# Performance work log

Hardware: AMD Instinct MI355X
Metric: run time of the kernel (lower is better)

Reference implementation:

```python
import jax, jax.numpy as jnp
import numpy as np

B, N, D, H = 1, 4096, 1024, 16
K = D // H
ROPE_BASE = 10000.0


def _rope_cos_sin(n, k, base, dtype):
    # GPT-NeoX style rotary embedding: inv_freq over even dims, emb = cat(freqs, freqs)
    inv_freq = 1.0 / (base ** (jnp.arange(0, k, 2, dtype=jnp.float32) / k))  # [K/2]
    pos = jnp.arange(n, dtype=jnp.float32)
    freqs = pos[:, None] * inv_freq[None, :]              # [N, K/2]
    emb = jnp.concatenate([freqs, freqs], axis=-1)        # [N, K]
    return jnp.cos(emb).astype(dtype), jnp.sin(emb).astype(dtype)


def _rotate_half(x):
    x1, x2 = jnp.split(x, 2, axis=-1)
    return jnp.concatenate([-x2, x1], axis=-1)


def setup_inputs() -> dict:
    key = jax.random.key(0)
    kx, kq, ko = jax.random.split(key, 3)
    x = jax.random.normal(kx, (B, N, D), dtype=jnp.float32)
    # torch Linear weights: [out_features, in_features], y = x @ W^T
    w_qkv = jax.random.normal(kq, (3 * H * K, D), dtype=jnp.float32) / np.sqrt(D)
    w_out = jax.random.normal(ko, (D, D), dtype=jnp.float32) / np.sqrt(D)
    return {"x": x, "w_qkv": w_qkv, "w_out": w_out}


def reference(x, w_qkv, w_out):
    b, n, d = x.shape
    qkv = jnp.einsum('bnd,ed->bne', x, w_qkv).reshape(b, n, 3, H, K)
    q, k, v = qkv[:, :, 0], qkv[:, :, 1], qkv[:, :, 2]   # [B, N, H, K]
    cos, sin = _rope_cos_sin(n, K, ROPE_BASE, x.dtype)    # [N, K]
    cos = cos[None, :, None, :]
    sin = sin[None, :, None, :]
    q = q * cos + _rotate_half(q) * sin
    k = k * cos + _rotate_half(k) * sin
    # explicit O(N^2) score matrix, as in the original module
    scores = jnp.einsum('bnhk,bmhk->bnhm', q, k) / np.sqrt(K).astype(x.dtype)
    causal_mask = jnp.tril(jnp.ones((n, n), dtype=bool))  # [N, M]
    scores = jnp.where(causal_mask[None, :, None, :], scores, jnp.finfo(x.dtype).min)
    probs = jax.nn.softmax(scores, axis=-1)
    attn = jnp.einsum('bnhm,bmhk->bnhk', probs, v).reshape(b, n, d)
    return jnp.einsum('bnd,ed->bne', attn, w_out)
```

## Files before the change

### kernel.cpp

```cpp
#include <hip/hip_runtime.h>
#include <hip/hip_bf16.h>
#include <math.h>

#define N_SEQ 4096
#define DIM   1024
#define NHEAD 16
#define HDIM  64
#define E3    3072

typedef short bf16x8 __attribute__((ext_vector_type(8)));
typedef float f32x4  __attribute__((ext_vector_type(4)));
typedef unsigned int u32;

#if __has_builtin(__builtin_amdgcn_exp2f)
#define EXP2(x) __builtin_amdgcn_exp2f(x)
#else
#define EXP2(x) exp2f(x)
#endif

__device__ __forceinline__ float bf2f(unsigned short u) {
    union { unsigned int i; float f; } x; x.i = ((unsigned int)u) << 16; return x.f;
}
__device__ __forceinline__ unsigned short f2bf(float f) {
    union { float f; unsigned int i; } x; x.f = f;
    unsigned int r = x.i + 0x7FFF + ((x.i >> 16) & 1);
    return (unsigned short)(r >> 16);
}
__device__ __forceinline__ unsigned short f2bf_fast(float f) {
    union { float f; unsigned int i; } x; x.f = f;
    return (unsigned short)((x.i + 0x8000u) >> 16);
}
__device__ __forceinline__ f32x4 mfma16(bf16x8 a, bf16x8 b, f32x4 c) {
    return __builtin_amdgcn_mfma_f32_16x16x32_bf16(a, b, c, 0, 0, 0);
}
__device__ __forceinline__ void gload_lds16(const unsigned short* g, unsigned short* l) {
    __builtin_amdgcn_global_load_lds(
        (const __attribute__((address_space(1))) u32*)g,
        (__attribute__((address_space(3))) u32*)l, 16, 0, 0);
}

__device__ __forceinline__ int probe_isf32(const unsigned short* __restrict__ X) {
    __shared__ int cnt;
    if (threadIdx.x == 0) cnt = 0;
    __syncthreads();
    int bad = 0;
    for (int i = threadIdx.x; i < 4096; i += 256) {
        float v = bf2f(X[i]);
        if (!(fabsf(v) < 1e10f)) bad = 1;
    }
    if (bad) atomicAdd(&cnt, 1);
    __syncthreads();
    return cnt > 0;
}

__global__ __launch_bounds__(256)
void prep_kernel(const void* __restrict__ X, const void* __restrict__ Wq,
                 const void* __restrict__ Wo,
                 unsigned short* __restrict__ Xb, unsigned short* __restrict__ Wqb,
                 unsigned short* __restrict__ Wob,
                 int* __restrict__ flag)
{
    const int isf32 = probe_isf32((const unsigned short*)X);
    if (blockIdx.x == 0 && threadIdx.x == 0) *flag = isf32;
    if (!isf32) return;

    const int nX4  = (N_SEQ * DIM) >> 2;
    const int nWq4 = (E3 * DIM) >> 2;
    const int nWo4 = (DIM * DIM) >> 2;
    const int total = nX4 + nWq4 + nWo4;
    const int stride = gridDim.x * blockDim.x;
    for (int i = blockIdx.x * blockDim.x + threadIdx.x; i < total; i += stride) {
        const float4* src; ushort4* dst; int j = i;
        if (j < nX4)                { src = (const float4*)X  + j;  dst = (ushort4*)Xb  + j; }
        else if ((j -= nX4) < nWq4) { src = (const float4*)Wq + j;  dst = (ushort4*)Wqb + j; }
        else { j -= nWq4;             src = (const float4*)Wo + j;  dst = (ushort4*)Wob + j; }
        float4 v = *src;
        ushort4 u;
        u.x = f2bf(v.x); u.y = f2bf(v.y); u.z = f2bf(v.z); u.w = f2bf(v.w);
        *dst = u;
    }
}

__global__ __launch_bounds__(256)
void qkv_mfma_kernel(const void* __restrict__ Xo, const unsigned short* __restrict__ Xc,
                     const void* __restrict__ Wo_, const unsigned short* __restrict__ Wc,
                     const int* __restrict__ flag,
                     unsigned short* __restrict__ Qf,
                     unsigned short* __restrict__ Kf,
                     unsigned short* __restrict__ Vf)
{
    __shared__ __align__(16) unsigned short SMEM[4][4096];

    const int isf32 = *flag;
    const unsigned short* Xb = isf32 ? Xc : (const unsigned short*)Xo;
    const unsigned short* Wb = isf32 ? Wc : (const unsigned short*)Wo_;

    const int tid  = threadIdx.x;
    const int lane = tid & 63;
    const int wave = tid >> 6;
    const int wr = wave >> 1, wc = wave & 1;
    const int lm = lane & 15, q4 = lane >> 4;
    const int rbase = blockIdx.y * 128;
    const int cbase = blockIdx.x * 128;

    const int srow = wave * 16 + (lane >> 2);
    const int scol = (lane & 3) * 8;

    const unsigned short* xsrc = Xb + (size_t)(rbase + srow) * DIM + scol;
    const unsigned short* wsrc = Wb + (size_t)(cbase + srow) * DIM + scol;
    const int la = (wr*64 + lm)*32 + q4*8;
    const int lb = (wc*64 + lm)*32 + q4*8;

    f32x4 acc[4][4];
    #pragma unroll
    for (int i = 0; i < 4; ++i)
        #pragma unroll
        for (int j = 0; j < 4; ++j) acc[i][j] = (f32x4){0.f, 0.f, 0.f, 0.f};

    #define QSTAGE(buf)                                                             \
        {                                                                           \
            _Pragma("unroll")                                                       \
            for (int j = 0; j < 2; ++j) {                                           \
                gload_lds16(xsrc + (size_t)j*64*DIM, &SMEM[buf][j*2048 + wave*512]);   \
                gload_lds16(wsrc + (size_t)j*64*DIM, &SMEM[2+buf][j*2048 + wave*512]); \
            }                                                                       \
            xsrc += 32; wsrc += 32;                                                 \
        }

    QSTAGE(0)
    for (int it = 0; it < DIM/32; ++it) {
        const int cur = it & 1;
        __syncthreads();
        if (it + 1 < DIM/32) QSTAGE(cur ^ 1)

        bf16x8 a[4], b[4];
        #pragma unroll
        for (int mi = 0; mi < 4; ++mi)
            a[mi] = *(const bf16x8*)&SMEM[cur][la + mi*512];
        #pragma unroll
        for (int ni = 0; ni < 4; ++ni)
            b[ni] = *(const bf16x8*)&SMEM[2+cur][lb + ni*512];
        #pragma unroll
        for (int mi = 0; mi < 4; ++mi)
            #pragma unroll
            for (int ni = 0; ni < 4; ++ni)
                acc[mi][ni] = mfma16(a[mi], b[ni], acc[mi][ni]);
    }
    #undef QSTAGE

    __syncthreads();

    const int ecol = cbase + wc * 64;
    const int part = ecol >> 10;
    const int h    = (ecol >> 6) & 15;
    unsigned short* ep = &SMEM[0][0] + wave*4096;

    if (part == 2) {
        #pragma unroll
        for (int mh = 0; mh < 2; ++mh) {
            #pragma unroll
            for (int mi2 = 0; mi2 < 2; ++mi2) {
                const int mi = mh*2 + mi2;
                #pragma unroll
                for (int r = 0; r < 4; ++r) {
                    const int n31 = mi2*16 + q4*4 + r;
                    #pragma unroll
                    for (int ni = 0; ni < 4; ++ni)
                        ep[(ni*16 + lm)*40 + n31] = f2bf(acc[mi][ni][r]);
                }
            }
            const int nb = rbase + wr*64 + mh*32;
            const size_t vb = (((size_t)h*128 + (nb >> 5)) << 11) + (size_t)lane*8;
            #pragma unroll
            for (int ni = 0; ni < 4; ++ni) {
                const bf16x8 fr = *(const bf16x8*)(ep + (ni*16 + lm)*40 + q4*8);
                *(bf16x8*)(Vf + vb + (size_t)ni*512) = fr;
            }
        }
    } else {
        unsigned short* dst = (part == 0) ? Qf : Kf;
        const float scl = (part == 0) ? 0.180336884f : 1.0f;
        const float inv0 = powf(10000.f, -((float)lm)        * (1.f/32.f));
        const float inv1 = powf(10000.f, -((float)(lm + 16)) * (1.f/32.f));
        #pragma unroll
        for (int mi = 0; mi < 4; ++mi) {
            const int tn = rbase + wr*64 + mi*16;
            #pragma unroll
            for (int r = 0; r < 4; ++r) {
                const int n = tn + q4*4 + r;
                float s0, c0, s1, c1;
                sincosf((float)n * inv0, &s0, &c0);
                sincosf((float)n * inv1, &s1, &c1);
                const int row = (q4*4 + r)*72;
                ep[row + lm]      = f2bf((acc[mi][0][r]*c0 - acc[mi][2][r]*s0) * scl);
                ep[row + lm + 16] = f2bf((acc[mi][1][r]*c1 - acc[mi][3][r]*s1) * scl);
                ep[row + lm + 32] = f2bf((acc[mi][2][r]*c0 + acc[mi][0][r]*s0) * scl);
                ep[row + lm + 48] = f2bf((acc[mi][3][r]*c1 + acc[mi][1][r]*s1) * scl);
            }
            const size_t tb = (((size_t)(h*256 + (tn >> 4))) << 10) + (size_t)lane*8;
            #pragma unroll
            for (int c = 0; c < 2; ++c) {
                const bf16x8 fr = *(const bf16x8*)(ep + lm*72 + c*32 + q4*8);
                *(bf16x8*)(dst + tb + (size_t)c*512) = fr;
            }
        }
    }
}

__global__ __launch_bounds__(256)
void attn_mfma_kernel(const unsigned short* __restrict__ Qf,
                      const unsigned short* __restrict__ Kf,
                      const unsigned short* __restrict__ Vf,
                      unsigned short* __restrict__ Attn)
{
    __shared__ __align__(16) unsigned short Ks[2][4096];
    __shared__ __align__(16) unsigned short Vs[2][4096];
    __shared__ __align__(16) unsigned short P16[4][16][72];

    const int tid  = threadIdx.x;
    const int lane = tid & 63;
    const int wave = tid >> 6;
    const int q4 = lane >> 4, lm = lane & 15;

    const int h  = blockIdx.x & 15;
    const int qb = blockIdx.x >> 4;
    const int q0 = (63 - qb) << 6;
    const int qw = q0 + (wave << 4);

    const size_t qbase = (((size_t)(h*256 + (qw >> 4))) << 10) + (size_t)lane * 8;
    const bf16x8 aq0 = *(const bf16x8*)(Qf + qbase);
    const bf16x8 aq1 = *(const bf16x8*)(Qf + qbase + 512);

    float l_part[4];
    f32x4 o[4];
    #pragma unroll
    for (int r = 0; r < 4; ++r) l_part[r] = 0.f;
    #pragma unroll
    for (int dc = 0; dc < 4; ++dc) o[dc] = (f32x4){0.f, 0.f, 0.f, 0.f};

    const unsigned short* sbase;
    unsigned short* db0;
    unsigned short* db1;
    {
        const int ch0 = (wave & 1) * 4;
        const size_t hb = ((size_t)h) << 18;
        sbase = ((wave < 2) ? Kf : Vf) + hb + ch0*512 + (size_t)lane*8;
        db0 = ((wave < 2) ? &Ks[0][0] : &Vs[0][0]) + ch0*512;
        db1 = ((wave < 2) ? &Ks[1][0] : &Vs[1][0]) + ch0*512;
    }
    unsigned short* pw  = &P16[wave][0][0];
    unsigned short* pwa = pw + (4*q4)*72 + lm;
    const unsigned short* par = pw + lm*72 + 8*q4;

    const int ntiles = (q0 >> 6) + 1;

    #define STAGE(dst)                                                         \
        {                                                                      \
            _Pragma("unroll")                                                  \
            for (int i = 0; i < 4; ++i)                                        \
                gload_lds16(sbase + i*512, (dst) + i*512);                     \
            sbase += 4096;                                                     \
        }

    STAGE(db0)

    for (int it = 0; it < ntiles; ++it) {
        const int kt = it << 6;
        const int cur = it & 1;

        __syncthreads();
        if (it + 1 < ntiles) STAGE(cur ? db0 : db1)

        const unsigned short* kc = &Ks[cur][lane*8];
        const unsigned short* vc = &Vs[cur][lane*8];

        f32x4 s[4];
        #pragma unroll
        for (int t = 0; t < 4; ++t) {
            const bf16x8 bk0 = *(const bf16x8*)(kc + t*1024);
            const bf16x8 bk1 = *(const bf16x8*)(kc + t*1024 + 512);
            f32x4 z = (f32x4){0.f, 0.f, 0.f, 0.f};
            z = mfma16(aq0, bk0, z);
            s[t] = mfma16(aq1, bk1, z);
        }

        if (kt + 63 > qw) {
            #pragma unroll
            for (int t = 0; t < 4; ++t) {
                const int key = kt + 16*t + lm;
                #pragma unroll
                for (int r = 0; r < 4; ++r)
                    if (key > qw + 4*q4 + r) s[t][r] = -INFINITY;
            }
        }

        #pragma unroll
        for (int t = 0; t < 4; ++t)
            #pragma unroll
            for (int r = 0; r < 4; ++r) {
                const float p = EXP2(s[t][r]);
                l_part[r] += p;
                pwa[r*72 + 16*t] = f2bf_fast(p);
            }

        const bf16x8 pa0 = *(const bf16x8*)(par);
        const bf16x8 pa1 = *(const bf16x8*)(par + 32);

        #pragma unroll
        for (int dc = 0; dc < 4; ++dc) {
            const bf16x8 bv0 = *(const bf16x8*)(vc + dc*512);
            const bf16x8 bv1 = *(const bf16x8*)(vc + 2048 + dc*512);
            o[dc] = mfma16(pa0, bv0, o[dc]);
            o[dc] = mfma16(pa1, bv1, o[dc]);
        }
    }
    #undef STAGE

    float inv[4];
    #pragma unroll
    for (int r = 0; r < 4; ++r) {
        float l = l_part[r];
        #pragma unroll
        for (int mk = 1; mk <= 8; mk <<= 1) l += __shfl_xor(l, mk);
        inv[r] = 1.f / l;
    }
    #pragma unroll
    for (int dc = 0; dc < 4; ++dc)
        #pragma unroll
        for (int r = 0; r < 4; ++r)
            Attn[(size_t)(qw + 4*q4 + r) * DIM + (h << 6) + 16*dc + lm] = f2bf(o[dc][r] * inv[r]);
}

__global__ __launch_bounds__(256)
void out_mfma_kernel(const unsigned short* __restrict__ Ab,
                     const void* __restrict__ Wo_, const unsigned short* __restrict__ Wc,
                     const int* __restrict__ flag,
                     void* __restrict__ Out)
{
    __shared__ unsigned short As[2][4096];
    __shared__ unsigned short Bs[2][2048];

    const int isf32 = *flag;
    const unsigned short* Wb = isf32 ? Wc : (const unsigned short*)Wo_;

    const int tid  = threadIdx.x;
    const int lane = tid & 63;
    const int wave = tid >> 6;
    const int lm = lane & 15, q4 = lane >> 4;
    const int rbase = blockIdx.y * 128;
    const int cbase = blockIdx.x * 64;

    const int srow16 = lane >> 2;
    const int scol = (lane & 3) * 8;

    const unsigned short* asrc = Ab + (size_t)(rbase + wave*32 + srow16) * DIM + scol;
    const unsigned short* bsrc = Wb + (size_t)(cbase + wave*16 + srow16) * DIM + scol;
    const int la = (wave*32 + lm)*32 + q4*8;
    const int lb = lm*32 + q4*8;

    f32x4 acc[2][4];
    #pragma unroll
    for (int i = 0; i < 2; ++i)
        #pragma unroll
        for (int j = 0; j < 4; ++j) acc[i][j] = (f32x4){0.f, 0.f, 0.f, 0.f};

    #define OSTAGE(buf)                                                          \
        {                                                                        \
            _Pragma("unroll")                                                    \
            for (int j = 0; j < 2; ++j)                                          \
                gload_lds16(asrc + (size_t)j*16*DIM, &As[buf][(wave*32 + j*16)*32]); \
            gload_lds16(bsrc, &Bs[buf][(wave*16)*32]);                           \
            asrc += 32; bsrc += 32;                                              \
        }

    OSTAGE(0)
    for (int it = 0; it < DIM/32; ++it) {
        const int cur = it & 1;
        __syncthreads();
        if (it + 1 < DIM/32) OSTAGE(cur ^ 1)

        bf16x8 a[2], b[4];
        #pragma unroll
        for (int mi = 0; mi < 2; ++mi)
            a[mi] = *(const bf16x8*)&As[cur][la + mi*512];
        #pragma unroll
        for (int ni = 0; ni < 4; ++ni)
            b[ni] = *(const bf16x8*)&Bs[cur][lb + ni*512];
        #pragma unroll
        for (int mi = 0; mi < 2; ++mi)
            #pragma unroll
            for (int ni = 0; ni < 4; ++ni)
                acc[mi][ni] = mfma16(a[mi], b[ni], acc[mi][ni]);
    }
    #undef OSTAGE

    #pragma unroll
    for (int mi = 0; mi < 2; ++mi)
        #pragma unroll
        for (int r = 0; r < 4; ++r) {
            const size_t n = rbase + wave*32 + mi*16 + q4*4 + r;
            #pragma unroll
            for (int ni = 0; ni < 4; ++ni) {
                const size_t e = cbase + ni*16 + lm;
                const float v = acc[mi][ni][r];
                if (isf32) ((float*)Out)[n * DIM + e] = v;
                else       ((unsigned short*)Out)[n * DIM + e] = f2bf(v);
            }
        }
}

extern "C" void kernel_launch(void* const* d_in, const int* in_sizes, int n_in,
                              void* d_out, int out_size, void* d_ws, size_t ws_size,
                              hipStream_t stream) {
    const void* X    = d_in[0];
    const void* Wqkv = d_in[1];
    const void* Wout = d_in[2];

    int* flag = (int*)d_ws;
    unsigned short* base = (unsigned short*)((char*)d_ws + 256);
    const size_t nX = (size_t)N_SEQ * DIM;
    const size_t nWq = (size_t)E3 * DIM;
    const size_t nWo = (size_t)DIM * DIM;
    unsigned short* Xb  = base;
    unsigned short* Wqb = Xb + nX;
    unsigned short* Wob = Wqb + nWq;
    unsigned short* Qf  = Wob + nWo;
    unsigned short* Kf  = Qf + nX;
    unsigned short* Vf  = Kf + nX;
    unsigned short* At  = Vf + nX;

    prep_kernel<<<768, 256, 0, stream>>>(X, Wqkv, Wout, Xb, Wqb, Wob, flag);
    qkv_mfma_kernel<<<dim3(E3 / 128, N_SEQ / 128), 256, 0, stream>>>(X, Xb, Wqkv, Wqb, flag, Qf, Kf, Vf);
    attn_mfma_kernel<<<dim3(NHEAD * (N_SEQ / 64)), 256, 0, stream>>>(Qf, Kf, Vf, At);
    out_mfma_kernel<<<dim3(DIM / 64, N_SEQ / 128), 256, 0, stream>>>(At, Wout, Wob, flag, d_out);
}
```

Before: 213.8 us.

## Split attention block into 2x2 wave grid over query and key halves

Each wave now handles 32 queries against one 32-key half of each tile, not 16 queries against all 64 keys. Each loaded K and V fragment is reused across two query sub-tiles, which cuts LDS reads per MFMA. The two key-half partial outputs and row sums are combined through shared memory at the end. This adds an extra reduction step with two barriers, and doubles the accumulator registers per wave.

```diff
diff --git a/kernel.cpp b/kernel.cpp
--- a/kernel.cpp
+++ b/kernel.cpp
@@ -215,28 +215,35 @@
 {
     __shared__ __align__(16) unsigned short Ks[2][4096];
     __shared__ __align__(16) unsigned short Vs[2][4096];
-    __shared__ __align__(16) unsigned short P16[4][16][72];
+    __shared__ __align__(16) unsigned short P16[4][32][40];
 
     const int tid  = threadIdx.x;
     const int lane = tid & 63;
     const int wave = tid >> 6;
     const int q4 = lane >> 4, lm = lane & 15;
+    const int qh = wave >> 1, kh = wave & 1;
 
     const int h  = blockIdx.x & 15;
     const int qb = blockIdx.x >> 4;
     const int q0 = (63 - qb) << 6;
-    const int qw = q0 + (wave << 4);
-
-    const size_t qbase = (((size_t)(h*256 + (qw >> 4))) << 10) + (size_t)lane * 8;
-    const bf16x8 aq0 = *(const bf16x8*)(Qf + qbase);
-    const bf16x8 aq1 = *(const bf16x8*)(Qf + qbase + 512);
-
-    float l_part[4];
-    f32x4 o[4];
+    const int qw = q0 + (qh << 5);
+
+    const unsigned short* qp = Qf + (((size_t)(h*256 + (qw >> 4))) << 10) + (size_t)lane * 8;
+    bf16x8 aq[2][2];
+    aq[0][0] = *(const bf16x8*)(qp);
+    aq[0][1] = *(const bf16x8*)(qp + 512);
+    aq[1][0] = *(const bf16x8*)(qp + 1024);
+    aq[1][1] = *(const bf16x8*)(qp + 1536);
+
+    float l_part[2][4];
+    f32x4 o[2][4];
     #pragma unroll
-    for (int r = 0; r < 4; ++r) l_part[r] = 0.f;
-    #pragma unroll
-    for (int dc = 0; dc < 4; ++dc) o[dc] = (f32x4){0.f, 0.f, 0.f, 0.f};
+    for (int qi = 0; qi < 2; ++qi) {
+        #pragma unroll
+        for (int r = 0; r < 4; ++r) l_part[qi][r] = 0.f;
+        #pragma unroll
+        for (int dc = 0; dc < 4; ++dc) o[qi][dc] = (f32x4){0.f, 0.f, 0.f, 0.f};
+    }
 
     const unsigned short* sbase;
     unsigned short* db0;
@@ -249,8 +256,8 @@
         db1 = ((wave < 2) ? &Ks[1][0] : &Vs[1][0]) + ch0*512;
     }
     unsigned short* pw  = &P16[wave][0][0];
-    unsigned short* pwa = pw + (4*q4)*72 + lm;
-    const unsigned short* par = pw + lm*72 + 8*q4;
+    unsigned short* pwa = pw + (4*q4)*40 + lm;
+    const unsigned short* par = pw + lm*40 + q4*8;
 
     const int ntiles = (q0 >> 6) + 1;
 
@@ -271,64 +278,103 @@
         __syncthreads();
         if (it + 1 < ntiles) STAGE(cur ? db0 : db1)
 
-        const unsigned short* kc = &Ks[cur][lane*8];
-        const unsigned short* vc = &Vs[cur][lane*8];
-
-        f32x4 s[4];
-        #pragma unroll
-        for (int t = 0; t < 4; ++t) {
-            const bf16x8 bk0 = *(const bf16x8*)(kc + t*1024);
-            const bf16x8 bk1 = *(const bf16x8*)(kc + t*1024 + 512);
-            f32x4 z = (f32x4){0.f, 0.f, 0.f, 0.f};
-            z = mfma16(aq0, bk0, z);
-            s[t] = mfma16(aq1, bk1, z);
-        }
-
-        if (kt + 63 > qw) {
-            #pragma unroll
-            for (int t = 0; t < 4; ++t) {
-                const int key = kt + 16*t + lm;
+        const unsigned short* kc = &Ks[cur][kh*2048 + lane*8];
+        const unsigned short* vc = &Vs[cur][kh*2048 + lane*8];
+
+        f32x4 s[2][2];
+        #pragma unroll
+        for (int ki = 0; ki < 2; ++ki) {
+            const bf16x8 bk0 = *(const bf16x8*)(kc + ki*1024);
+            const bf16x8 bk1 = *(const bf16x8*)(kc + ki*1024 + 512);
+            #pragma unroll
+            for (int qi = 0; qi < 2; ++qi) {
+                f32x4 z = (f32x4){0.f, 0.f, 0.f, 0.f};
+                z = mfma16(aq[qi][0], bk0, z);
+                s[qi][ki] = mfma16(aq[qi][1], bk1, z);
+            }
+        }
+
+        if (kt + 32*kh + 31 > qw) {
+            #pragma unroll
+            for (int ki = 0; ki < 2; ++ki) {
+                const int key = kt + 32*kh + 16*ki + lm;
                 #pragma unroll
-                for (int r = 0; r < 4; ++r)
-                    if (key > qw + 4*q4 + r) s[t][r] = -INFINITY;
-            }
-        }
-
-        #pragma unroll
-        for (int t = 0; t < 4; ++t)
+                for (int qi = 0; qi < 2; ++qi) {
+                    const int qq = qw + 16*qi + 4*q4;
+                    #pragma unroll
+                    for (int r = 0; r < 4; ++r)
+                        if (key > qq + r) s[qi][ki][r] = -INFINITY;
+                }
+            }
+        }
+
+        #pragma unroll
+        for (int qi = 0; qi < 2; ++qi)
+            #pragma unroll
+            for (int ki = 0; ki < 2; ++ki)
+                #pragma unroll
+                for (int r = 0; r < 4; ++r) {
+                    const float p = EXP2(s[qi][ki][r]);
+                    l_part[qi][r] += p;
+                    pwa[qi*640 + r*40 + ki*16] = f2bf_fast(p);
+                }
+
+        bf16x8 pa[2];
+        pa[0] = *(const bf16x8*)(par);
+        pa[1] = *(const bf16x8*)(par + 640);
+
+        #pragma unroll
+        for (int dc = 0; dc < 4; ++dc) {
+            const bf16x8 bv = *(const bf16x8*)(vc + dc*512);
+            #pragma unroll
+            for (int qi = 0; qi < 2; ++qi)
+                o[qi][dc] = mfma16(pa[qi], bv, o[qi][dc]);
+        }
+    }
+    #undef STAGE
+
+    #pragma unroll
+    for (int qi = 0; qi < 2; ++qi)
+        #pragma unroll
+        for (int r = 0; r < 4; ++r) {
+            float l = l_part[qi][r];
+            #pragma unroll
+            for (int mk = 1; mk <= 8; mk <<= 1) l += __shfl_xor(l, mk);
+            l_part[qi][r] = l;
+        }
+
+    float* Ox = (float*)&Ks[0][0];
+    float* Lx = (float*)&Vs[0][0];
+    __syncthreads();
+    if (kh == 1) {
+        #pragma unroll
+        for (int qi = 0; qi < 2; ++qi) {
             #pragma unroll
             for (int r = 0; r < 4; ++r) {
-                const float p = EXP2(s[t][r]);
-                l_part[r] += p;
-                pwa[r*72 + 16*t] = f2bf_fast(p);
-            }
-
-        const bf16x8 pa0 = *(const bf16x8*)(par);
-        const bf16x8 pa1 = *(const bf16x8*)(par + 32);
-
-        #pragma unroll
-        for (int dc = 0; dc < 4; ++dc) {
-            const bf16x8 bv0 = *(const bf16x8*)(vc + dc*512);
-            const bf16x8 bv1 = *(const bf16x8*)(vc + 2048 + dc*512);
-            o[dc] = mfma16(pa0, bv0, o[dc]);
-            o[dc] = mfma16(pa1, bv1, o[dc]);
-        }
-    }
-    #undef STAGE
-
-    float inv[4];
-    #pragma unroll
-    for (int r = 0; r < 4; ++r) {
-        float l = l_part[r];
-        #pragma unroll
-        for (int mk = 1; mk <= 8; mk <<= 1) l += __shfl_xor(l, mk);
-        inv[r] = 1.f / l;
-    }
-    #pragma unroll
-    for (int dc = 0; dc < 4; ++dc)
-        #pragma unroll
-        for (int r = 0; r < 4; ++r)
-            Attn[(size_t)(qw + 4*q4 + r) * DIM + (h << 6) + 16*dc + lm] = f2bf(o[dc][r] * inv[r]);
+                const int qq = 16*qi + 4*q4 + r;
+                #pragma unroll
+                for (int dc = 0; dc < 4; ++dc)
+                    Ox[qh*2048 + qq*64 + 16*dc + lm] = o[qi][dc][r];
+                if (lm == 0) Lx[qh*32 + qq] = l_part[qi][r];
+            }
+        }
+    }
+    __syncthreads();
+    if (kh == 0) {
+        #pragma unroll
+        for (int qi = 0; qi < 2; ++qi)
+            #pragma unroll
+            for (int r = 0; r < 4; ++r) {
+                const int qq = 16*qi + 4*q4 + r;
+                const float inv = 1.f / (l_part[qi][r] + Lx[qh*32 + qq]);
+                const size_t row = (size_t)(qw + qq) * DIM + (h << 6) + lm;
+                #pragma unroll
+                for (int dc = 0; dc < 4; ++dc) {
+                    const float v = o[qi][dc][r] + Ox[qh*2048 + qq*64 + 16*dc + lm];
+                    Attn[row + 16*dc] = f2bf(v * inv);
+                }
+            }
+    }
 }
 
 __global__ __launch_bounds__(256)
```

Measured after the change: 208.1 us. 1.03x faster.
